# Kernel optimization log

Measured on AMD Instinct MI355X. Metric: run time of the kernel, lower is better.

The kernel has to match this reference:

```python
import jax, jax.numpy as jnp
import numpy as np

N = 100_000            # nodes
E = 1_600_000          # edges per metapath
IN = 256               # input features
HEADS, DIM = 8, 16     # heads * dim = hidden_channels
HIDDEN = HEADS * DIM   # 128
OUT = 4                # classes
NEG_SLOPE = 0.2


def setup_inputs() -> dict:
    key = jax.random.key(0)
    ks = jax.random.split(key, 16)
    s = 1.0 / np.sqrt(HIDDEN)
    return {
        "x": jax.random.normal(ks[0], (N, IN), jnp.float32),
        "edge_index0": jax.random.randint(ks[1], (2, E), 0, N, jnp.int64),
        "edge_index1": jax.random.randint(ks[2], (2, E), 0, N, jnp.int64),
        "proj_w": jax.random.normal(ks[3], (IN, HIDDEN), jnp.float32) / np.sqrt(IN),
        "proj_b": jnp.zeros((HIDDEN,), jnp.float32),
        "att_src0": jax.random.normal(ks[4], (HEADS, DIM), jnp.float32) * s,
        "att_dst0": jax.random.normal(ks[5], (HEADS, DIM), jnp.float32) * s,
        "att_src1": jax.random.normal(ks[6], (HEADS, DIM), jnp.float32) * s,
        "att_dst1": jax.random.normal(ks[7], (HEADS, DIM), jnp.float32) * s,
        "k_lin_w": jax.random.normal(ks[8], (HIDDEN, HIDDEN), jnp.float32) * s,
        "k_lin_b": jnp.zeros((HIDDEN,), jnp.float32),
        "q": jax.random.normal(ks[9], (HIDDEN,), jnp.float32) * s,
        "lin_w": jax.random.normal(ks[10], (HIDDEN, OUT), jnp.float32) * s,
        "lin_b": jnp.zeros((OUT,), jnp.float32),
    }


def _metapath_conv(xp, a_src, a_dst, src, dst):
    # xp: [N,H,D]; a_src, a_dst: [H,D]; src/dst: [E]
    alpha_src = (xp * a_src).sum(-1)                     # [N,H]
    alpha_dst = (xp * a_dst).sum(-1)                     # [N,H]
    e = jax.nn.leaky_relu(alpha_src[src] + alpha_dst[dst], NEG_SLOPE)  # [E,H]
    emax = jax.ops.segment_max(e, dst, num_segments=N)  # [N,H] (stable softmax)
    e = jnp.exp(e - emax[dst])
    denom = jax.ops.segment_sum(e, dst, num_segments=N)
    alpha = e / (denom[dst] + 1e-16)                     # edge softmax per dst
    msg = xp[src] * alpha[..., None]                     # [E,H,D]
    out = jax.ops.segment_sum(msg, dst, num_segments=N)  # [N,H,D]
    return jax.nn.relu(out.reshape(N, HIDDEN))


def reference(x, edge_index0, edge_index1, proj_w, proj_b,
              att_src0, att_dst0, att_src1, att_dst1,
              k_lin_w, k_lin_b, q, lin_w, lin_b):
    # shared node-type projection
    xp = (x @ proj_w + proj_b).reshape(N, HEADS, DIM)
    # per-metapath GAT-style convolutions (dropout=0.6 is eval no-op)
    outs = jnp.stack([
        _metapath_conv(xp, att_src0, att_dst0, edge_index0[0], edge_index0[1]),
        _metapath_conv(xp, att_src1, att_dst1, edge_index1[0], edge_index1[1]),
    ])                                                    # [M,N,HIDDEN]
    # semantic attention over metapaths
    k = jnp.tanh(outs @ k_lin_w + k_lin_b).mean(axis=1)  # [M,HIDDEN]
    attn = jax.nn.softmax((k * q).sum(-1))               # [M]
    fused = (attn[:, None, None] * outs).sum(0)          # [N,HIDDEN]
    return fused @ lin_w + lin_b                          # [N,OUT]
```

## Files before the change

kernel.cpp:

```cpp
#include <hip/hip_runtime.h>
#include <hip/hip_bf16.h>

#define NN 100000
#define EE 1600000
#define HID 128
#define NEG 0.2f
#define CAP 64
#define BSH 9
#define NB 196
#define CAPB 9216
#define EBLK 4096

typedef __attribute__((ext_vector_type(8))) short short8;
typedef __attribute__((ext_vector_type(4))) float f32x4;

static __device__ __forceinline__ float bf2f(short s) {
  union { float f; unsigned u; } c;
  c.u = ((unsigned)(unsigned short)s) << 16;
  return c.f;
}

#define PWS 264
#define PNT ((NN + 15) / 16)
#define PGX 512

__global__ __launch_bounds__(256) void k_proj(const float* __restrict__ x,
    const float* __restrict__ w, const float* __restrict__ bias,
    const float* __restrict__ a0s, const float* __restrict__ a0d,
    const float* __restrict__ a1s, const float* __restrict__ a1d,
    __hip_bfloat16* __restrict__ xph,
    float* __restrict__ as0, float* __restrict__ ad0,
    float* __restrict__ as1, float* __restrict__ ad1) {
  __shared__ short wT[128 * PWS];
  const int tid = threadIdx.x;
  for (int l = tid; l < 256 * 128; l += 256) {
    int k = l >> 7, n = l & 127;
    __hip_bfloat16 bv = __float2bfloat16(w[l]);
    wT[n * PWS + k] = *(short*)&bv;
  }
  const int lane = tid & 63, wave = tid >> 6;
  const int rowgrp = lane >> 4, lcol = lane & 15;
  float bv[8], A0S[8], A0D[8], A1S[8], A1D[8];
#pragma unroll
  for (int ct = 0; ct < 8; ct++) {
    bv[ct] = bias[ct * 16 + lcol];
    A0S[ct] = a0s[ct * 16 + lcol];
    A0D[ct] = a0d[ct * 16 + lcol];
    A1S[ct] = a1s[ct * 16 + lcol];
    A1D[ct] = a1d[ct * 16 + lcol];
  }
  __syncthreads();
  for (int tile = blockIdx.x * 4 + wave; tile < PNT; tile += gridDim.x * 4) {
    const int r0 = tile * 16;
    int row = r0 + lcol;
    if (row >= NN) row = NN - 1;
    const float* xr = x + (size_t)row * 256 + rowgrp * 8;
    short8 af[8];
#pragma unroll
    for (int kc = 0; kc < 8; kc++) {
      float4 u0 = *(const float4*)(xr + kc * 32);
      float4 u1 = *(const float4*)(xr + kc * 32 + 4);
      union { short8 v; __hip_bfloat162 h[4]; } u;
      u.h[0] = __float22bfloat162_rn(make_float2(u0.x, u0.y));
      u.h[1] = __float22bfloat162_rn(make_float2(u0.z, u0.w));
      u.h[2] = __float22bfloat162_rn(make_float2(u1.x, u1.y));
      u.h[3] = __float22bfloat162_rn(make_float2(u1.z, u1.w));
      af[kc] = u.v;
    }
#pragma unroll
    for (int ct = 0; ct < 8; ct++) {
      f32x4 acc = {0.f, 0.f, 0.f, 0.f};
#pragma unroll
      for (int kc = 0; kc < 8; kc++) {
        short8 bf = *(const short8*)&wT[(ct * 16 + lcol) * PWS + kc * 32 + rowgrp * 8];
        acc = __builtin_amdgcn_mfma_f32_16x16x32_bf16(af[kc], bf, acc, 0, 0, 0);
      }
#pragma unroll
      for (int r = 0; r < 4; r++) {
        int orow = r0 + rowgrp * 4 + r;
        float xv = acc[r] + bv[ct];
        if (orow < NN) {
          __hip_bfloat16 ob = __float2bfloat16(xv);
          ((short*)xph)[(size_t)orow * 128 + ct * 16 + lcol] = *(short*)&ob;
        }
        float q0 = xv * A0S[ct], q1 = xv * A0D[ct], q2 = xv * A1S[ct], q3 = xv * A1D[ct];
#pragma unroll
        for (int off = 1; off < 16; off <<= 1) {
          q0 += __shfl_xor(q0, off, 64);
          q1 += __shfl_xor(q1, off, 64);
          q2 += __shfl_xor(q2, off, 64);
          q3 += __shfl_xor(q3, off, 64);
        }
        if (lcol == 0 && orow < NN) {
          as0[orow * 8 + ct] = q0;
          ad0[orow * 8 + ct] = q1;
          as1[orow * 8 + ct] = q2;
          ad1[orow * 8 + ct] = q3;
        }
      }
    }
  }
}

__global__ __launch_bounds__(256) void k_bin(const int* __restrict__ ei0,
    const int* __restrict__ ei1, int* __restrict__ gcur, int* __restrict__ binned) {
  const int p = blockIdx.y;
  const int* __restrict__ ei = p ? ei1 : ei0;
  const int* __restrict__ src = ei;
  const int* __restrict__ dst = ei + EE;
  int* __restrict__ gc = gcur + p * 256;
  int* __restrict__ bn = binned + (size_t)p * NB * CAPB;
  __shared__ int cntL[NB], baseL[NB], posL[NB];
  const int t = threadIdx.x;
  const int e0 = blockIdx.x * EBLK;
  const int e1 = min(e0 + EBLK, EE);
  for (int i = t; i < NB; i += 256) { cntL[i] = 0; posL[i] = 0; }
  __syncthreads();
  for (int e = e0 + t; e < e1; e += 256)
    atomicAdd(&cntL[dst[e] >> BSH], 1);
  __syncthreads();
  for (int i = t; i < NB; i += 256)
    baseL[i] = atomicAdd(&gc[i], cntL[i]);
  __syncthreads();
  for (int e = e0 + t; e < e1; e += 256) {
    int d = dst[e];
    int b = d >> BSH;
    int off = baseL[b] + atomicAdd(&posL[b], 1);
    if (off < CAPB) bn[b * CAPB + off] = (src[e] << BSH) | (d & 511);
  }
}

__global__ __launch_bounds__(512) void k_build(const int* __restrict__ gcur,
    const int* __restrict__ binned, int* __restrict__ cnt, int* __restrict__ csr) {
  const int p = blockIdx.y, b = blockIdx.x, t = threadIdx.x;
  const int* __restrict__ bn = binned + (size_t)p * NB * CAPB + (size_t)b * CAPB;
  const int n = min(gcur[p * 256 + b], CAPB);
  int* __restrict__ cs = csr + (size_t)p * NN * CAP;
  __shared__ int lc[512];
  lc[t] = 0;
  __syncthreads();
  const int node0 = b << BSH;
  for (int i = t; i < n; i += 512) {
    int v = bn[i];
    int ln = v & 511;
    int off = atomicAdd(&lc[ln], 1);
    if (off < CAP) cs[(size_t)(node0 + ln) * CAP + off] = v >> BSH;
  }
  __syncthreads();
  int n0 = node0 + t;
  if (n0 < NN) cnt[p * NN + n0] = lc[t];
}


#define EDGE_BODY(sv)                                      \
  {                                                        \
    unsigned s = (unsigned)(sv);                           \
    float t = asrc[s * 8u + h];                            \
    __hip_bfloat162 v = xph[s * 64u + lane];               \
    float tt = t + ad;                                     \
    float al = __expf(fmaxf(tt, NEG * tt));                \
    denom += al;                                           \
    float2 f = __bfloat1622float2(v);                      \
    a0 = fmaf(al, f.x, a0);                                \
    a1 = fmaf(al, f.y, a1);                                \
  }

__global__ __launch_bounds__(256) void k_aggr(const __hip_bfloat162* __restrict__ xph,
    const float* __restrict__ as0, const float* __restrict__ ad0,
    const float* __restrict__ as1, const float* __restrict__ ad1,
    const int* __restrict__ cnt, const int* __restrict__ csr,
    __hip_bfloat162* __restrict__ h0, __hip_bfloat162* __restrict__ h1) {
  const int p = blockIdx.y;
  const unsigned lane = threadIdx.x & 63;
  int node = blockIdx.x * 4 + (threadIdx.x >> 6);
  if (node >= NN) return;
  node = __builtin_amdgcn_readfirstlane(node);
  const float* __restrict__ asrc = p ? as1 : as0;
  const float* __restrict__ adst = p ? ad1 : ad0;
  const int* __restrict__ cs = csr + ((size_t)p * NN + node) * CAP;
  __hip_bfloat162* __restrict__ hout = p ? h1 : h0;
  const unsigned h = lane >> 3;
  const float ad = adst[(unsigned)node * 8u + h];
  const int deg = min(cnt[p * NN + node], CAP);

  float denom = 1e-16f, a0 = 0.f, a1 = 0.f;
  int e = 0;
  for (; e + 8 <= deg; e += 8) {
    int4 q0 = *(const int4*)&cs[e];
    int4 q1 = *(const int4*)&cs[e + 4];
    EDGE_BODY(q0.x) EDGE_BODY(q0.y) EDGE_BODY(q0.z) EDGE_BODY(q0.w)
    EDGE_BODY(q1.x) EDGE_BODY(q1.y) EDGE_BODY(q1.z) EDGE_BODY(q1.w)
  }
  for (; e + 4 <= deg; e += 4) {
    int4 q0 = *(const int4*)&cs[e];
    EDGE_BODY(q0.x) EDGE_BODY(q0.y) EDGE_BODY(q0.z) EDGE_BODY(q0.w)
  }
  for (; e < deg; e++) EDGE_BODY(cs[e])
  float inv = 1.f / denom;
  hout[(size_t)node * 64 + lane] =
      __float22bfloat162_rn(make_float2(fmaxf(a0 * inv, 0.f), fmaxf(a1 * inv, 0.f)));
}

#define KWS 136
#define NTILES ((NN + 63) / 64)
#define SEMGX 512

__global__ __launch_bounds__(256) void k_sem(const __hip_bfloat16* __restrict__ h0,
    const __hip_bfloat16* __restrict__ h1, const float* __restrict__ kw,
    const float* __restrict__ kb, const float* __restrict__ lw,
    float* __restrict__ ksum, float* __restrict__ o0, float* __restrict__ o1) {
  __shared__ short kwT[128 * KWS];
  __shared__ float red[4][128];
  __shared__ float lwS[512];
  const int tid = threadIdx.x;
  const int m = blockIdx.y;
  const short* __restrict__ hc = (const short*)(m ? h1 : h0);
  float* __restrict__ oc = m ? o1 : o0;
  for (int l = tid; l < 128 * 128; l += 256) {
    int i = l >> 7, j = l & 127;
    __hip_bfloat16 bv = __float2bfloat16(kw[l]);
    kwT[j * KWS + i] = *(short*)&bv;
  }
  for (int l = tid; l < 512; l += 256) lwS[l] = lw[l];
  const int lane = tid & 63;
  const int wave = tid >> 6;
  const int rowgrp = lane >> 4;
  const int lcol = lane & 15;
  float partial[8] = {};
  float kbv[8];
#pragma unroll
  for (int ct = 0; ct < 8; ct++) kbv[ct] = kb[ct * 16 + lcol];
  __syncthreads();
  for (int tile = blockIdx.x; tile < NTILES; tile += SEMGX) {
    int n0 = tile * 64 + wave * 16;
    int row = n0 + lcol;
    if (row >= NN) row = 0;
    const short* hr = hc + (size_t)row * 128 + rowgrp * 8;
    short8 afrag[4];
#pragma unroll
    for (int kc = 0; kc < 4; kc++) afrag[kc] = *(const short8*)(hr + kc * 32);
    float op[4] = {0.f, 0.f, 0.f, 0.f};
#pragma unroll
    for (int kc = 0; kc < 4; kc++) {
      union { short8 v; short s[8]; } u;
      u.v = afrag[kc];
#pragma unroll
      for (int j = 0; j < 8; j++) {
        float hv = bf2f(u.s[j]);
        const float4 lv = *(const float4*)&lwS[(kc * 32 + rowgrp * 8 + j) * 4];
        op[0] = fmaf(hv, lv.x, op[0]);
        op[1] = fmaf(hv, lv.y, op[1]);
        op[2] = fmaf(hv, lv.z, op[2]);
        op[3] = fmaf(hv, lv.w, op[3]);
      }
    }
#pragma unroll
    for (int c = 0; c < 4; c++) {
      op[c] += __shfl_xor(op[c], 16, 64);
      op[c] += __shfl_xor(op[c], 32, 64);
    }
    int orow = n0 + lcol;
    if (rowgrp == 0 && orow < NN) {
      float4 ov = make_float4(op[0], op[1], op[2], op[3]);
      *(float4*)&oc[(size_t)orow * 4] = ov;
    }
#pragma unroll
    for (int ct = 0; ct < 8; ct++) {
      f32x4 acc = {0.f, 0.f, 0.f, 0.f};
#pragma unroll
      for (int kc = 0; kc < 4; kc++) {
        short8 bfrag = *(const short8*)&kwT[(ct * 16 + lcol) * KWS + kc * 32 + rowgrp * 8];
        acc = __builtin_amdgcn_mfma_f32_16x16x32_bf16(afrag[kc], bfrag, acc, 0, 0, 0);
      }
#pragma unroll
      for (int r = 0; r < 4; r++) {
        int node = n0 + rowgrp * 4 + r;
        if (node < NN) partial[ct] += tanhf(acc[r] + kbv[ct]);
      }
    }
  }
#pragma unroll
  for (int ct = 0; ct < 8; ct++) {
    partial[ct] += __shfl_xor(partial[ct], 16, 64);
    partial[ct] += __shfl_xor(partial[ct], 32, 64);
  }
  if (lane < 16) {
#pragma unroll
    for (int ct = 0; ct < 8; ct++) red[wave][ct * 16 + lane] = partial[ct];
  }
  __syncthreads();
  if (tid < 128) {
    float s = red[0][tid] + red[1][tid] + red[2][tid] + red[3][tid];
    atomicAdd(&ksum[m * 128 + tid], s);
  }
}

__global__ void k_attn(const float* __restrict__ ksum, const float* __restrict__ q,
                       float* __restrict__ attn) {
  __shared__ float red0[128], red1[128];
  int t = threadIdx.x;
  float qv = q[t];
  red0[t] = ksum[t] * qv;
  red1[t] = ksum[128 + t] * qv;
  __syncthreads();
  for (int off = 64; off > 0; off >>= 1) {
    if (t < off) {
      red0[t] += red0[t + off];
      red1[t] += red1[t + off];
    }
    __syncthreads();
  }
  if (t == 0) {
    float l0 = red0[0] / (float)NN, l1 = red1[0] / (float)NN;
    float mx = fmaxf(l0, l1);
    float e0 = __expf(l0 - mx), e1 = __expf(l1 - mx);
    float s = e0 + e1;
    attn[0] = e0 / s;
    attn[1] = e1 / s;
  }
}

__global__ __launch_bounds__(256) void k_blend(const float* __restrict__ o0,
    const float* __restrict__ o1, const float* __restrict__ lb,
    const float* __restrict__ attn, float* __restrict__ out) {
  int i = blockIdx.x * 256 + threadIdx.x;
  if (i >= NN * 4) return;
  out[i] = attn[0] * o0[i] + attn[1] * o1[i] + lb[i & 3];
}

extern "C" void kernel_launch(void* const* d_in, const int* in_sizes, int n_in,
                              void* d_out, int out_size, void* d_ws, size_t ws_size,
                              hipStream_t stream) {
  const float* x      = (const float*)d_in[0];
  const int*   ei0    = (const int*)d_in[1];
  const int*   ei1    = (const int*)d_in[2];
  const float* proj_w = (const float*)d_in[3];
  const float* proj_b = (const float*)d_in[4];
  const float* a0s    = (const float*)d_in[5];
  const float* a0d    = (const float*)d_in[6];
  const float* a1s    = (const float*)d_in[7];
  const float* a1d    = (const float*)d_in[8];
  const float* klw    = (const float*)d_in[9];
  const float* klb    = (const float*)d_in[10];
  const float* q      = (const float*)d_in[11];
  const float* lw     = (const float*)d_in[12];
  const float* lb     = (const float*)d_in[13];
  float* out = (float*)d_out;

  char* ws = (char*)d_ws;
  size_t off = 0;
  auto alloc = [&](size_t bytes) -> void* {
    size_t o = (off + 255) & ~(size_t)255;
    off = o + bytes;
    return (void*)(ws + o);
  };
  __hip_bfloat162* xph = (__hip_bfloat162*)alloc((size_t)NN * 128 * 2);
  __hip_bfloat162* h0  = (__hip_bfloat162*)alloc((size_t)NN * 128 * 2);
  __hip_bfloat162* h1  = (__hip_bfloat162*)alloc((size_t)NN * 128 * 2);
  float* as0  = (float*)alloc((size_t)NN * 8 * 4);
  float* ad0  = (float*)alloc((size_t)NN * 8 * 4);
  float* as1  = (float*)alloc((size_t)NN * 8 * 4);
  float* ad1  = (float*)alloc((size_t)NN * 8 * 4);
  int* cnt    = (int*)alloc((size_t)2 * NN * 4);
  float* ksum = (float*)alloc(256 * 4);
  int* gcur   = (int*)alloc(2 * 256 * 4);
  float* attn = (float*)alloc(256);
  int* csr    = (int*)alloc((size_t)2 * NN * CAP * 4);
  int* binned = (int*)alloc((size_t)2 * NB * CAPB * 4);
  float* o0   = (float*)alloc((size_t)NN * 4 * 4);
  float* o1   = (float*)alloc((size_t)NN * 4 * 4);

  hipMemsetAsync(cnt, 0, (size_t)2 * NN * 4 + 256 * 4 + 2 * 256 * 4, stream);

  k_proj<<<dim3(PGX), 256, 0, stream>>>(x, proj_w, proj_b, a0s, a0d, a1s, a1d,
                                        (__hip_bfloat16*)xph, as0, ad0, as1, ad1);
  k_bin<<<dim3((EE + EBLK - 1) / EBLK, 2), 256, 0, stream>>>(ei0, ei1, gcur, binned);
  k_build<<<dim3(NB, 2), 512, 0, stream>>>(gcur, binned, cnt, csr);
  k_aggr<<<dim3((NN + 3) / 4, 2), 256, 0, stream>>>(xph, as0, ad0, as1, ad1,
                                                    cnt, csr, h0, h1);
  k_sem<<<dim3(SEMGX, 2), 256, 0, stream>>>((const __hip_bfloat16*)h0,
                                            (const __hip_bfloat16*)h1, klw, klb, lw,
                                            ksum, o0, o1);
  k_attn<<<dim3(1), 128, 0, stream>>>(ksum, q, attn);
  k_blend<<<dim3((NN * 4 + 255) / 256), 256, 0, stream>>>(o0, o1, lb, attn, out);
}
```

Measured before the change: 526.4 us.

## Replace binned CSR build with direct atomics and pretranspose weights once

Replaces the two-pass binned edge bucketing (k_bin + k_build) with a single kernel that places each edge into the per-destination CSR through global atomics. Also moves the bf16 weight transposes into a one-off prep kernel so the projection and semantic kernels read pre-transposed weights from global memory instead of rebuilding them in LDS in every block. Further changes: the attention logits are pre-scaled by log2(e) so the edge path can use a raw v_exp_f32, tanh uses a fast exp2/rcp form, the four attention-score reductions are merged into one shuffle tree, and k_attn is folded into k_blend. The direct atomics cause contention on random destinations and make neighbor order nondeterministic, and the fast transcendentals lose a little accuracy.

```diff
diff --git a/kernel.cpp b/kernel.cpp
--- a/kernel.cpp
+++ b/kernel.cpp
@@ -6,10 +6,7 @@
 #define HID 128
 #define NEG 0.2f
 #define CAP 64
-#define BSH 9
-#define NB 196
-#define CAPB 9216
-#define EBLK 4096
+#define EPB 8192
 
 typedef __attribute__((ext_vector_type(8))) short short8;
 typedef __attribute__((ext_vector_type(4))) float f32x4;
@@ -20,36 +17,61 @@
   return c.f;
 }
 
-#define PWS 264
+static __device__ __forceinline__ float exp2_fast(float x) {
+  float r;
+  asm("v_exp_f32 %0, %1" : "=v"(r) : "v"(x));
+  return r;
+}
+
+static __device__ __forceinline__ float tanh_fast(float x) {
+  float a = fminf(fmaxf(x * 2.885390082f, -40.f), 40.f);
+  float e = exp2_fast(a);
+  float r = __builtin_amdgcn_rcpf(e + 1.f);
+  return fmaf(-2.f, r, 1.f);
+}
+
+__global__ __launch_bounds__(256) void k_wprep(const float* __restrict__ w,
+    const float* __restrict__ kw, short* __restrict__ wTg, short* __restrict__ kwTg) {
+  int i = blockIdx.x * 256 + threadIdx.x;
+  if (i < 32768) {
+    int n = i >> 8, k = i & 255;
+    __hip_bfloat16 b = __float2bfloat16(w[k * 128 + n]);
+    wTg[i] = *(short*)&b;
+  } else if (i < 49152) {
+    int j = i - 32768;
+    int n = j >> 7, k = j & 127;
+    __hip_bfloat16 b = __float2bfloat16(kw[k * 128 + n]);
+    kwTg[j] = *(short*)&b;
+  }
+}
+
 #define PNT ((NN + 15) / 16)
-#define PGX 512
+#define PGX 782
 
 __global__ __launch_bounds__(256) void k_proj(const float* __restrict__ x,
-    const float* __restrict__ w, const float* __restrict__ bias,
+    const short* __restrict__ wTg, const float* __restrict__ bias,
     const float* __restrict__ a0s, const float* __restrict__ a0d,
     const float* __restrict__ a1s, const float* __restrict__ a1d,
     __hip_bfloat16* __restrict__ xph,
     float* __restrict__ as0, float* __restrict__ ad0,
     float* __restrict__ as1, float* __restrict__ ad1) {
-  __shared__ short wT[128 * PWS];
   const int tid = threadIdx.x;
-  for (int l = tid; l < 256 * 128; l += 256) {
-    int k = l >> 7, n = l & 127;
-    __hip_bfloat16 bv = __float2bfloat16(w[l]);
-    wT[n * PWS + k] = *(short*)&bv;
-  }
   const int lane = tid & 63, wave = tid >> 6;
   const int rowgrp = lane >> 4, lcol = lane & 15;
-  float bv[8], A0S[8], A0D[8], A1S[8], A1D[8];
+  const bool b3 = (lcol & 8) != 0, b2 = (lcol & 4) != 0;
+  const int ttype = (lcol >> 2) & 3;
+  float* __restrict__ ap = (ttype == 0) ? as0 : (ttype == 1) ? ad0
+                         : (ttype == 2) ? as1 : ad1;
+  float bv[8], AS0[8], AD0[8], AS1[8], AD1[8];
+  const float L2E = 1.44269504f;
 #pragma unroll
   for (int ct = 0; ct < 8; ct++) {
     bv[ct] = bias[ct * 16 + lcol];
-    A0S[ct] = a0s[ct * 16 + lcol];
-    A0D[ct] = a0d[ct * 16 + lcol];
-    A1S[ct] = a1s[ct * 16 + lcol];
-    A1D[ct] = a1d[ct * 16 + lcol];
-  }
-  __syncthreads();
+    AS0[ct] = a0s[ct * 16 + lcol] * L2E;
+    AD0[ct] = a0d[ct * 16 + lcol] * L2E;
+    AS1[ct] = a1s[ct * 16 + lcol] * L2E;
+    AD1[ct] = a1d[ct * 16 + lcol] * L2E;
+  }
   for (int tile = blockIdx.x * 4 + wave; tile < PNT; tile += gridDim.x * 4) {
     const int r0 = tile * 16;
     int row = r0 + lcol;
@@ -72,7 +94,7 @@
       f32x4 acc = {0.f, 0.f, 0.f, 0.f};
 #pragma unroll
       for (int kc = 0; kc < 8; kc++) {
-        short8 bf = *(const short8*)&wT[(ct * 16 + lcol) * PWS + kc * 32 + rowgrp * 8];
+        short8 bf = *(const short8*)&wTg[(ct * 16 + lcol) * 256 + kc * 32 + rowgrp * 8];
         acc = __builtin_amdgcn_mfma_f32_16x16x32_bf16(af[kc], bf, acc, 0, 0, 0);
       }
 #pragma unroll
@@ -83,72 +105,37 @@
           __hip_bfloat16 ob = __float2bfloat16(xv);
           ((short*)xph)[(size_t)orow * 128 + ct * 16 + lcol] = *(short*)&ob;
         }
-        float q0 = xv * A0S[ct], q1 = xv * A0D[ct], q2 = xv * A1S[ct], q3 = xv * A1D[ct];
-#pragma unroll
-        for (int off = 1; off < 16; off <<= 1) {
-          q0 += __shfl_xor(q0, off, 64);
-          q1 += __shfl_xor(q1, off, 64);
-          q2 += __shfl_xor(q2, off, 64);
-          q3 += __shfl_xor(q3, off, 64);
-        }
-        if (lcol == 0 && orow < NN) {
-          as0[orow * 8 + ct] = q0;
-          ad0[orow * 8 + ct] = q1;
-          as1[orow * 8 + ct] = q2;
-          ad1[orow * 8 + ct] = q3;
-        }
-      }
-    }
-  }
-}
-
-__global__ __launch_bounds__(256) void k_bin(const int* __restrict__ ei0,
-    const int* __restrict__ ei1, int* __restrict__ gcur, int* __restrict__ binned) {
+        float q0 = xv * AS0[ct], q1 = xv * AD0[ct], q2 = xv * AS1[ct], q3 = xv * AD1[ct];
+        float va = (b3 ? q2 : q0) + __shfl_xor(b3 ? q0 : q2, 8, 64);
+        float vb = (b3 ? q3 : q1) + __shfl_xor(b3 ? q1 : q3, 8, 64);
+        float v  = (b2 ? vb : va) + __shfl_xor(b2 ? va : vb, 4, 64);
+        v += __shfl_xor(v, 2, 64);
+        v += __shfl_xor(v, 1, 64);
+        if ((lcol & 3) == 0 && orow < NN) ap[orow * 8 + ct] = v;
+      }
+    }
+  }
+}
+
+__global__ __launch_bounds__(256) void k_edges(const int* __restrict__ ei0,
+    const int* __restrict__ ei1, int* __restrict__ cnt, int* __restrict__ csr) {
   const int p = blockIdx.y;
   const int* __restrict__ ei = p ? ei1 : ei0;
   const int* __restrict__ src = ei;
   const int* __restrict__ dst = ei + EE;
-  int* __restrict__ gc = gcur + p * 256;
-  int* __restrict__ bn = binned + (size_t)p * NB * CAPB;
-  __shared__ int cntL[NB], baseL[NB], posL[NB];
-  const int t = threadIdx.x;
-  const int e0 = blockIdx.x * EBLK;
-  const int e1 = min(e0 + EBLK, EE);
-  for (int i = t; i < NB; i += 256) { cntL[i] = 0; posL[i] = 0; }
-  __syncthreads();
-  for (int e = e0 + t; e < e1; e += 256)
-    atomicAdd(&cntL[dst[e] >> BSH], 1);
-  __syncthreads();
-  for (int i = t; i < NB; i += 256)
-    baseL[i] = atomicAdd(&gc[i], cntL[i]);
-  __syncthreads();
-  for (int e = e0 + t; e < e1; e += 256) {
-    int d = dst[e];
-    int b = d >> BSH;
-    int off = baseL[b] + atomicAdd(&posL[b], 1);
-    if (off < CAPB) bn[b * CAPB + off] = (src[e] << BSH) | (d & 511);
-  }
-}
-
-__global__ __launch_bounds__(512) void k_build(const int* __restrict__ gcur,
-    const int* __restrict__ binned, int* __restrict__ cnt, int* __restrict__ csr) {
-  const int p = blockIdx.y, b = blockIdx.x, t = threadIdx.x;
-  const int* __restrict__ bn = binned + (size_t)p * NB * CAPB + (size_t)b * CAPB;
-  const int n = min(gcur[p * 256 + b], CAPB);
+  int* __restrict__ cn = cnt + p * NN;
   int* __restrict__ cs = csr + (size_t)p * NN * CAP;
-  __shared__ int lc[512];
-  lc[t] = 0;
-  __syncthreads();
-  const int node0 = b << BSH;
-  for (int i = t; i < n; i += 512) {
-    int v = bn[i];
-    int ln = v & 511;
-    int off = atomicAdd(&lc[ln], 1);
-    if (off < CAP) cs[(size_t)(node0 + ln) * CAP + off] = v >> BSH;
-  }
-  __syncthreads();
-  int n0 = node0 + t;
-  if (n0 < NN) cnt[p * NN + n0] = lc[t];
+  const int e0 = blockIdx.x * EPB;
+  const int e1 = min(e0 + EPB, EE);
+  for (int e = e0 + threadIdx.x * 4; e + 4 <= e1; e += 1024) {
+    int4 d4 = *(const int4*)&dst[e];
+    int4 s4 = *(const int4*)&src[e];
+    int o;
+    o = atomicAdd(&cn[d4.x], 1); if (o < CAP) cs[(size_t)d4.x * CAP + o] = s4.x;
+    o = atomicAdd(&cn[d4.y], 1); if (o < CAP) cs[(size_t)d4.y * CAP + o] = s4.y;
+    o = atomicAdd(&cn[d4.z], 1); if (o < CAP) cs[(size_t)d4.z * CAP + o] = s4.z;
+    o = atomicAdd(&cn[d4.w], 1); if (o < CAP) cs[(size_t)d4.w * CAP + o] = s4.w;
+  }
 }
 
 
@@ -158,7 +145,7 @@
     float t = asrc[s * 8u + h];                            \
     __hip_bfloat162 v = xph[s * 64u + lane];               \
     float tt = t + ad;                                     \
-    float al = __expf(fmaxf(tt, NEG * tt));                \
+    float al = exp2_fast(fmaxf(tt, NEG * tt));             \
     denom += al;                                           \
     float2 f = __bfloat1622float2(v);                      \
     a0 = fmaf(al, f.x, a0);                                \
@@ -201,26 +188,19 @@
       __float22bfloat162_rn(make_float2(fmaxf(a0 * inv, 0.f), fmaxf(a1 * inv, 0.f)));
 }
 
-#define KWS 136
 #define NTILES ((NN + 63) / 64)
-#define SEMGX 512
+#define SEMGX 391
 
 __global__ __launch_bounds__(256) void k_sem(const __hip_bfloat16* __restrict__ h0,
-    const __hip_bfloat16* __restrict__ h1, const float* __restrict__ kw,
+    const __hip_bfloat16* __restrict__ h1, const short* __restrict__ kwTg,
     const float* __restrict__ kb, const float* __restrict__ lw,
     float* __restrict__ ksum, float* __restrict__ o0, float* __restrict__ o1) {
-  __shared__ short kwT[128 * KWS];
   __shared__ float red[4][128];
   __shared__ float lwS[512];
   const int tid = threadIdx.x;
   const int m = blockIdx.y;
   const short* __restrict__ hc = (const short*)(m ? h1 : h0);
   float* __restrict__ oc = m ? o1 : o0;
-  for (int l = tid; l < 128 * 128; l += 256) {
-    int i = l >> 7, j = l & 127;
-    __hip_bfloat16 bv = __float2bfloat16(kw[l]);
-    kwT[j * KWS + i] = *(short*)&bv;
-  }
   for (int l = tid; l < 512; l += 256) lwS[l] = lw[l];
   const int lane = tid & 63;
   const int wave = tid >> 6;
@@ -269,13 +249,13 @@
       f32x4 acc = {0.f, 0.f, 0.f, 0.f};
 #pragma unroll
       for (int kc = 0; kc < 4; kc++) {
-        short8 bfrag = *(const short8*)&kwT[(ct * 16 + lcol) * KWS + kc * 32 + rowgrp * 8];
+        short8 bfrag = *(const short8*)&kwTg[(ct * 16 + lcol) * 128 + kc * 32 + rowgrp * 8];
         acc = __builtin_amdgcn_mfma_f32_16x16x32_bf16(afrag[kc], bfrag, acc, 0, 0, 0);
       }
 #pragma unroll
       for (int r = 0; r < 4; r++) {
         int node = n0 + rowgrp * 4 + r;
-        if (node < NN) partial[ct] += tanhf(acc[r] + kbv[ct]);
+        if (node < NN) partial[ct] += tanh_fast(acc[r] + kbv[ct]);
       }
     }
   }
@@ -295,37 +275,34 @@
   }
 }
 
-__global__ void k_attn(const float* __restrict__ ksum, const float* __restrict__ q,
-                       float* __restrict__ attn) {
-  __shared__ float red0[128], red1[128];
-  int t = threadIdx.x;
-  float qv = q[t];
-  red0[t] = ksum[t] * qv;
-  red1[t] = ksum[128 + t] * qv;
-  __syncthreads();
-  for (int off = 64; off > 0; off >>= 1) {
-    if (t < off) {
-      red0[t] += red0[t + off];
-      red1[t] += red1[t + off];
-    }
-    __syncthreads();
-  }
-  if (t == 0) {
-    float l0 = red0[0] / (float)NN, l1 = red1[0] / (float)NN;
-    float mx = fmaxf(l0, l1);
-    float e0 = __expf(l0 - mx), e1 = __expf(l1 - mx);
-    float s = e0 + e1;
-    attn[0] = e0 / s;
-    attn[1] = e1 / s;
-  }
-}
-
 __global__ __launch_bounds__(256) void k_blend(const float* __restrict__ o0,
     const float* __restrict__ o1, const float* __restrict__ lb,
-    const float* __restrict__ attn, float* __restrict__ out) {
-  int i = blockIdx.x * 256 + threadIdx.x;
-  if (i >= NN * 4) return;
-  out[i] = attn[0] * o0[i] + attn[1] * o1[i] + lb[i & 3];
+    const float* __restrict__ ksum, const float* __restrict__ q,
+    float* __restrict__ out) {
+  __shared__ float aw[2];
+  const int t = threadIdx.x;
+  if (t < 64) {
+    float qa = q[t], qb = q[t + 64];
+    float s0 = fmaf(ksum[t], qa, ksum[t + 64] * qb);
+    float s1 = fmaf(ksum[128 + t], qa, ksum[192 + t] * qb);
+#pragma unroll
+    for (int off = 1; off < 64; off <<= 1) {
+      s0 += __shfl_xor(s0, off, 64);
+      s1 += __shfl_xor(s1, off, 64);
+    }
+    if (t == 0) {
+      float l0 = s0 * (1.f / NN), l1 = s1 * (1.f / NN);
+      float mx = fmaxf(l0, l1);
+      float e0 = __expf(l0 - mx), e1 = __expf(l1 - mx);
+      float inv = 1.f / (e0 + e1);
+      aw[0] = e0 * inv;
+      aw[1] = e1 * inv;
+    }
+  }
+  __syncthreads();
+  int i = blockIdx.x * 256 + t;
+  if (i < NN * 4)
+    out[i] = aw[0] * o0[i] + aw[1] * o1[i] + lb[i & 3];
 }
 
 extern "C" void kernel_launch(void* const* d_in, const int* in_sizes, int n_in,
@@ -363,24 +340,22 @@
   float* ad1  = (float*)alloc((size_t)NN * 8 * 4);
   int* cnt    = (int*)alloc((size_t)2 * NN * 4);
   float* ksum = (float*)alloc(256 * 4);
-  int* gcur   = (int*)alloc(2 * 256 * 4);
-  float* attn = (float*)alloc(256);
   int* csr    = (int*)alloc((size_t)2 * NN * CAP * 4);
-  int* binned = (int*)alloc((size_t)2 * NB * CAPB * 4);
+  short* wTg  = (short*)alloc(32768 * 2);
+  short* kwTg = (short*)alloc(16384 * 2);
   float* o0   = (float*)alloc((size_t)NN * 4 * 4);
   float* o1   = (float*)alloc((size_t)NN * 4 * 4);
 
-  hipMemsetAsync(cnt, 0, (size_t)2 * NN * 4 + 256 * 4 + 2 * 256 * 4, stream);
-
-  k_proj<<<dim3(PGX), 256, 0, stream>>>(x, proj_w, proj_b, a0s, a0d, a1s, a1d,
+  hipMemsetAsync(cnt, 0, (size_t)2 * NN * 4 + 256 * 4, stream);
+
+  k_wprep<<<dim3(192), 256, 0, stream>>>(proj_w, klw, wTg, kwTg);
+  k_proj<<<dim3(PGX), 256, 0, stream>>>(x, wTg, proj_b, a0s, a0d, a1s, a1d,
                                         (__hip_bfloat16*)xph, as0, ad0, as1, ad1);
-  k_bin<<<dim3((EE + EBLK - 1) / EBLK, 2), 256, 0, stream>>>(ei0, ei1, gcur, binned);
-  k_build<<<dim3(NB, 2), 512, 0, stream>>>(gcur, binned, cnt, csr);
+  k_edges<<<dim3((EE + EPB - 1) / EPB, 2), 256, 0, stream>>>(ei0, ei1, cnt, csr);
   k_aggr<<<dim3((NN + 3) / 4, 2), 256, 0, stream>>>(xph, as0, ad0, as1, ad1,
                                                     cnt, csr, h0, h1);
   k_sem<<<dim3(SEMGX, 2), 256, 0, stream>>>((const __hip_bfloat16*)h0,
-                                            (const __hip_bfloat16*)h1, klw, klb, lw,
+                                            (const __hip_bfloat16*)h1, kwTg, klb, lw,
                                             ksum, o0, o1);
-  k_attn<<<dim3(1), 128, 0, stream>>>(ksum, q, attn);
-  k_blend<<<dim3((NN * 4 + 255) / 256), 256, 0, stream>>>(o0, o1, lb, attn, out);
-}
+  k_blend<<<dim3((NN * 4 + 255) / 256), 256, 0, stream>>>(o0, o1, lb, ksum, q, out);
+}
```

Result: slower. 693.3 us (+31.7%).
